# Optimization experiments

Measured on AMD Instinct MI355X. Metric: run time of the kernel, lower is better.

The kernel has to match this reference:

```python
import jax, jax.numpy as jnp
import numpy as np

B, S, D, H = 4, 2048, 1024, 16
DEPTH = D // H


def setup_inputs() -> dict:
    key = jax.random.key(0)
    ks = jax.random.split(key, 12)
    q = jax.random.normal(ks[0], (B, S, D), dtype=jnp.float32)
    k = jax.random.normal(ks[1], (B, S, D), dtype=jnp.float32)
    v = jax.random.normal(ks[2], (B, S, D), dtype=jnp.float32)
    # causal mask: 1.0 where attention is disallowed (upper triangle), per `mask * -1e9`
    mask = 1.0 - jnp.tril(jnp.ones((S, S), dtype=jnp.float32))
    mask = mask[None, None, :, :]  # [1,1,S,S] broadcastable over batch/heads
    scale = 1.0 / np.sqrt(D)
    Wq = jax.random.normal(ks[3], (D, D), dtype=jnp.float32) * scale
    Wk = jax.random.normal(ks[4], (D, D), dtype=jnp.float32) * scale
    Wv = jax.random.normal(ks[5], (D, D), dtype=jnp.float32) * scale
    Wo = jax.random.normal(ks[6], (D, D), dtype=jnp.float32) * scale
    bq = jnp.zeros((D,), jnp.float32)
    bk = jnp.zeros((D,), jnp.float32)
    bv = jnp.zeros((D,), jnp.float32)
    bo = jnp.zeros((D,), jnp.float32)
    return {"query": q, "key": k, "value": v, "mask": mask,
            "Wq": Wq, "bq": bq, "Wk": Wk, "bk": bk,
            "Wv": Wv, "bv": bv, "Wo": Wo, "bo": bo}


def _split_heads(x):
    # [B, S, D] -> [B, H, S, depth]
    b, s, _ = x.shape
    return x.reshape(b, s, H, DEPTH).transpose(0, 2, 1, 3)


def reference(query, key, value, mask, Wq, bq, Wk, bk, Wv, bv, Wo, bo):
    q = _split_heads(query @ Wq + bq)   # [B,H,S,depth]
    k = _split_heads(key @ Wk + bk)
    v = _split_heads(value @ Wv + bv)
    scores = jnp.einsum('bhqd,bhkd->bhqk', q, k) / jnp.sqrt(
        jnp.asarray(DEPTH, q.dtype))
    scores = scores + mask * (-1e9)
    attn = jax.nn.softmax(scores, axis=-1)
    out = jnp.einsum('bhqk,bhkd->bhqd', attn, v)   # [B,H,S,depth]
    out = out.transpose(0, 2, 1, 3).reshape(query.shape[0], -1, H * DEPTH)
    return out @ Wo + bo
```

## Files before the change

kernel.cpp:

```cpp
#include <hip/hip_runtime.h>

#define Bsz 4
#define SEQ 2048
#define DIM 1024
#define NH 16
#define HD 64

typedef float  f32x4  __attribute__((ext_vector_type(4)));
typedef __bf16 bf16x8 __attribute__((ext_vector_type(8)));
typedef __bf16 bf16x4 __attribute__((ext_vector_type(4)));
typedef short  s16x4  __attribute__((ext_vector_type(4)));

__device__ __forceinline__ f32x4 mfma16(bf16x8 a, bf16x8 b, f32x4 c) {
    return __builtin_amdgcn_mfma_f32_16x16x32_bf16(a, b, c, 0, 0, 0);
}
__device__ __forceinline__ f32x4 mfma16k16(bf16x4 a, bf16x4 b, f32x4 c) {
#if defined(__has_builtin) && __has_builtin(__builtin_amdgcn_mfma_f32_16x16x16bf16_1k)
    return __builtin_amdgcn_mfma_f32_16x16x16bf16_1k(
        __builtin_bit_cast(s16x4, a), __builtin_bit_cast(s16x4, b), c, 0, 0, 0);
#else
    asm volatile("s_nop 2\n\tv_mfma_f32_16x16x16_bf16 %0, %1, %2, %0\n\ts_nop 7\n\ts_nop 7"
                 : "+v"(c) : "v"(a), "v"(b));
    return c;
#endif
}

#define GLD_LDS16(gsrc, ldst)                                                        \
    __builtin_amdgcn_global_load_lds(                                                \
        (const __attribute__((address_space(1))) void*)(gsrc),                       \
        (__attribute__((address_space(3))) void*)(ldst), 16, 0, 0)

__global__ __launch_bounds__(256) void wt_kernel(
    const float* __restrict__ Wq, const float* __restrict__ Wk,
    const float* __restrict__ Wv, const float* __restrict__ Wo,
    __bf16* __restrict__ wt)
{
    __shared__ float tile[64][65];
    int z = blockIdx.z;
    const float* W = (z == 0) ? Wq : (z == 1) ? Wk : (z == 2) ? Wv : Wo;
    __bf16* out = wt + (size_t)z * DIM * DIM;
    int kb = blockIdx.x * 64, nb = blockIdx.y * 64;
    int t = threadIdx.x;
    int cidx = t & 63, ridx = t >> 6;
#pragma unroll
    for (int i = 0; i < 16; i++) {
        int r = ridx + i * 4;
        tile[r][cidx] = W[(size_t)(kb + r) * DIM + nb + cidx];
    }
    __syncthreads();
#pragma unroll
    for (int i = 0; i < 16; i++) {
        int r = ridx + i * 4;
        out[(size_t)(nb + r) * DIM + kb + cidx] = (__bf16)tile[cidx][r];
    }
}

__global__ __launch_bounds__(256, 2) void gemm_proj(
    const float* __restrict__ Xq, const float* __restrict__ Xk,
    const float* __restrict__ Xv, const __bf16* __restrict__ wt,
    const float* __restrict__ bq, const float* __restrict__ bk,
    const float* __restrict__ bv,
    __bf16* __restrict__ oq, __bf16* __restrict__ ok, __bf16* __restrict__ ovT)
{
    int z = blockIdx.z;
    const float*  X    = (z == 0) ? Xq : (z == 1) ? Xk : Xv;
    const float*  bias = (z == 0) ? bq : (z == 1) ? bk : bv;
    const __bf16* Bt   = wt + (size_t)z * DIM * DIM;

    __shared__ __align__(16) char smem[36864];
    __bf16* const Ab = (__bf16*)smem;
    __bf16* const Bb = (__bf16*)(smem + 16384);

    int m0 = blockIdx.x * 128, n0 = blockIdx.y * 128;
    int tid = threadIdx.x, lane = tid & 63, w = tid >> 6;
    int c = lane & 15, g = lane >> 4;
    int wm = (w >> 1) * 64, wn = (w & 1) * 64;

    f32x4 acc[4][4] = {};

    int ar = tid >> 1, ah = tid & 1;
    const float* aptr = X + (size_t)(m0 + ar) * DIM + ah * 16;
    int awo = ar * 32 + ah * 16;

    int brow0 = (w * 2) * 16 + (lane >> 2);
    int bcol  = (lane & 3) * 8;
    const __bf16* bptr0 = Bt + (size_t)(n0 + brow0) * DIM + bcol;
    const __bf16* bptr1 = bptr0 + (size_t)16 * DIM;
    int bwo0 = (w * 2) * 512;
    int bwo1 = (w * 2 + 1) * 512;

    {
        f32x4 f0 = *(const f32x4*)(aptr);
        f32x4 f1 = *(const f32x4*)(aptr + 4);
        f32x4 f2 = *(const f32x4*)(aptr + 8);
        f32x4 f3 = *(const f32x4*)(aptr + 12);
        GLD_LDS16(bptr0, Bb + bwo0);
        GLD_LDS16(bptr1, Bb + bwo1);
        bf16x8 b0, b1;
#pragma unroll
        for (int j = 0; j < 4; j++) {
            b0[j]     = (__bf16)f0[j];
            b0[4 + j] = (__bf16)f1[j];
            b1[j]     = (__bf16)f2[j];
            b1[4 + j] = (__bf16)f3[j];
        }
        *(bf16x8*)(Ab + awo)     = b0;
        *(bf16x8*)(Ab + awo + 8) = b1;
    }
    __syncthreads();

    int cur = 0;
    for (int kt = 0; kt < 32; ++kt) {
        int nxt = kt + 1;
        int nb = cur ^ 1;
        f32x4 f0, f1, f2, f3;
        if (nxt < 32) {
            const float* ap = aptr + nxt * 32;
            f0 = *(const f32x4*)(ap);
            f1 = *(const f32x4*)(ap + 4);
            f2 = *(const f32x4*)(ap + 8);
            f3 = *(const f32x4*)(ap + 12);
            GLD_LDS16(bptr0 + nxt * 32, Bb + nb * 4096 + bwo0);
            GLD_LDS16(bptr1 + nxt * 32, Bb + nb * 4096 + bwo1);
        }
        bf16x8 af[4], bf[4];
#pragma unroll
        for (int mf = 0; mf < 4; mf++)
            af[mf] = *(bf16x8*)&Ab[cur * 4096 + (wm + mf * 16 + c) * 32 + g * 8];
#pragma unroll
        for (int nf = 0; nf < 4; nf++)
            bf[nf] = *(bf16x8*)&Bb[cur * 4096 + (wn + nf * 16 + c) * 32 + g * 8];
#pragma unroll
        for (int mf = 0; mf < 4; mf++)
#pragma unroll
            for (int nf = 0; nf < 4; nf++)
                acc[mf][nf] = mfma16(af[mf], bf[nf], acc[mf][nf]);
        if (nxt < 32) {
            bf16x8 b0, b1;
#pragma unroll
            for (int j = 0; j < 4; j++) {
                b0[j]     = (__bf16)f0[j];
                b0[4 + j] = (__bf16)f1[j];
                b1[j]     = (__bf16)f2[j];
                b1[4 + j] = (__bf16)f3[j];
            }
            *(bf16x8*)(Ab + nb * 4096 + awo)     = b0;
            *(bf16x8*)(Ab + nb * 4096 + awo + 8) = b1;
        }
        __syncthreads();
        cur = nb;
    }

    if (z == 2) {
        __bf16* T = (__bf16*)smem + (size_t)w * 4608;
#pragma unroll
        for (int nf = 0; nf < 4; nf++) {
            int col = n0 + wn + nf * 16 + c;
            int d = nf * 16 + c;
            float bval = bias[col];
#pragma unroll
            for (int mf = 0; mf < 4; mf++) {
                int sl = mf * 16 + g * 4;
                bf16x4 pk;
#pragma unroll
                for (int r = 0; r < 4; r++) pk[r] = (__bf16)(acc[mf][nf][r] + bval);
                *(bf16x4*)&T[d * 72 + sl] = pk;
            }
        }
        int h = (n0 + wn) >> 6;
        int bb = m0 >> 11;
        int s_base = (m0 & (SEQ - 1)) + wm;
        int dd = lane >> 2;
        int ss = (lane & 3) * 8;
        size_t obase = ((size_t)(bb * NH + h) * HD) * SEQ;
#pragma unroll
        for (int dgrp = 0; dgrp < 4; dgrp++)
#pragma unroll
            for (int half = 0; half < 2; half++) {
                int d = dgrp * 16 + dd;
                int s = half * 32 + ss;
                bf16x8 vv = *(bf16x8*)&T[d * 72 + s];
                *(bf16x8*)&ovT[obase + (size_t)d * SEQ + s_base + s] = vv;
            }
    } else {
        __bf16* Out = (z == 0) ? oq : ok;
#pragma unroll
        for (int nf = 0; nf < 4; nf++) {
            int col = n0 + wn + nf * 16 + c;
            float bval = bias[col];
#pragma unroll
            for (int mf = 0; mf < 4; mf++) {
                int row = m0 + wm + mf * 16 + g * 4;
#pragma unroll
                for (int r = 0; r < 4; r++)
                    Out[(size_t)(row + r) * DIM + col] = (__bf16)(acc[mf][nf][r] + bval);
            }
        }
    }
}

#define QSCALE 0.180336880f

__global__ __launch_bounds__(256, 2) void fa_kernel(
    const __bf16* __restrict__ qp, const __bf16* __restrict__ kp,
    const __bf16* __restrict__ vpT, __bf16* __restrict__ op)
{
    int bz = blockIdx.x;
    int bh = bz & 63;
    int b = bh >> 4, h = bh & 15;
    int qt = 15 - (bz >> 6);
    int q0 = qt * 128;

    int tid = threadIdx.x, lane = tid & 63, w = tid >> 6;
    int c = lane & 15, g = lane >> 4;

    __shared__ __bf16 Kbuf[64 * 64];
    __shared__ __bf16 Vbuf[64 * 64];

    const int qb[2] = {q0 + w * 16, q0 + 64 + w * 16};

    bf16x8 qf[2][2];
#pragma unroll
    for (int nq = 0; nq < 2; nq++) {
        const __bf16* qbase = qp + (size_t)(b * SEQ + qb[nq] + c) * DIM + h * HD;
#pragma unroll
        for (int kc = 0; kc < 2; kc++) {
            bf16x8 raw = *(const bf16x8*)(qbase + kc * 32 + g * 8);
            bf16x8 sc;
#pragma unroll
            for (int j = 0; j < 8; j++) sc[j] = (__bf16)((float)raw[j] * QSCALE);
            qf[nq][kc] = sc;
        }
    }

    f32x4 acc[4][2] = {};
    float m_run[2] = {-1e30f, -1e30f};
    float l_run[2] = {0.f, 0.f};

    int r8 = tid >> 3, c8 = tid & 7;
    int sch = c8 ^ (r8 & 7);
    const __bf16* kbase = kp  + (size_t)(b * SEQ + r8) * DIM + h * HD + sch * 8;
    const __bf16* vbase = vpT + ((size_t)(b * NH + h) * HD + r8) * SEQ + sch * 8;
    __bf16* kdst0 = Kbuf + w * 512;
    __bf16* kdst1 = Kbuf + 2048 + w * 512;
    __bf16* vdst0 = Vbuf + w * 512;
    __bf16* vdst1 = Vbuf + 2048 + w * 512;

    int vb4[4];
#pragma unroll
    for (int mkey = 0; mkey < 4; mkey++)
        vb4[mkey] = c * 64 + (((2 * mkey + (g >> 1)) ^ (c & 7)) * 8) + (g & 1) * 4;

    int ktmax = (q0 >> 6) + 2;
    for (int kt = 0; kt < ktmax; ++kt) {
        GLD_LDS16(kbase + (size_t)kt * 64 * DIM, kdst0);
        GLD_LDS16(kbase + (size_t)(kt * 64 + 32) * DIM, kdst1);
        GLD_LDS16(vbase + kt * 64, vdst0);
        GLD_LDS16(vbase + kt * 64 + (size_t)32 * SEQ, vdst1);
        __syncthreads();

        bool need0 = (kt * 64 <= qb[0] + 15);
        int kb0 = kt * 64;

        f32x4 s[4][2] = {};
#pragma unroll
        for (int kc = 0; kc < 2; kc++) {
            bf16x8 kf[4];
#pragma unroll
            for (int mkey = 0; mkey < 4; mkey++)
                kf[mkey] = *(bf16x8*)&Kbuf[(mkey * 16 + c) * 64 + (((kc * 4 + g) ^ (c & 7)) * 8)];
#pragma unroll
            for (int mkey = 0; mkey < 4; mkey++) {
                if (need0) s[mkey][0] = mfma16(kf[mkey], qf[0][kc], s[mkey][0]);
                s[mkey][1] = mfma16(kf[mkey], qf[1][kc], s[mkey][1]);
            }
        }

        bf16x4 pf[4][2];
#pragma unroll
        for (int nq = 0; nq < 2; nq++) {
            if (nq == 0 && !need0) continue;
            int qg = qb[nq] + c;
            if (kb0 + 63 > qg) {
#pragma unroll
                for (int mkey = 0; mkey < 4; mkey++)
#pragma unroll
                    for (int r2 = 0; r2 < 4; r2++)
                        if (kb0 + mkey * 16 + g * 4 + r2 > qg) s[mkey][nq][r2] = -1e30f;
            }
            float pm0 = fmaxf(fmaxf(s[0][nq][0], s[0][nq][1]), fmaxf(s[0][nq][2], s[0][nq][3]));
            float pm1 = fmaxf(fmaxf(s[1][nq][0], s[1][nq][1]), fmaxf(s[1][nq][2], s[1][nq][3]));
            float pm2 = fmaxf(fmaxf(s[2][nq][0], s[2][nq][1]), fmaxf(s[2][nq][2], s[2][nq][3]));
            float pm3 = fmaxf(fmaxf(s[3][nq][0], s[3][nq][1]), fmaxf(s[3][nq][2], s[3][nq][3]));
            float pm = fmaxf(fmaxf(pm0, pm1), fmaxf(pm2, pm3));
            pm = fmaxf(pm, __shfl_xor(pm, 16));
            pm = fmaxf(pm, __shfl_xor(pm, 32));
            float mo = m_run[nq];
            float mn = fmaxf(mo, pm);
            m_run[nq] = mn;
            float scl = exp2f(mo - mn);
            l_run[nq] *= scl;
#pragma unroll
            for (int nf = 0; nf < 4; nf++) acc[nf][nq] *= scl;
            float rs = 0.f;
#pragma unroll
            for (int mkey = 0; mkey < 4; mkey++) {
                bf16x4 pk;
#pragma unroll
                for (int r2 = 0; r2 < 4; r2++) {
                    float p = exp2f(s[mkey][nq][r2] - mn);
                    rs += p;
                    pk[r2] = (__bf16)p;
                }
                pf[mkey][nq] = pk;
            }
            rs += __shfl_xor(rs, 16);
            rs += __shfl_xor(rs, 32);
            l_run[nq] += rs;
        }

#pragma unroll
        for (int mkey = 0; mkey < 4; mkey++) {
#pragma unroll
            for (int nf = 0; nf < 4; nf++) {
                bf16x4 vf = *(bf16x4*)&Vbuf[vb4[mkey] + nf * 1024];
                if (need0) acc[nf][0] = mfma16k16(vf, pf[mkey][0], acc[nf][0]);
                acc[nf][1] = mfma16k16(vf, pf[mkey][1], acc[nf][1]);
            }
        }
        __syncthreads();
    }

#pragma unroll
    for (int nq = 0; nq < 2; nq++) {
        float inv = 1.f / l_run[nq];
        int row = qb[nq] + c;
        __bf16* obase = op + (size_t)(b * SEQ + row) * DIM + h * HD + g * 4;
#pragma unroll
        for (int nf = 0; nf < 4; nf++) {
            bf16x4 pk;
#pragma unroll
            for (int r2 = 0; r2 < 4; r2++) pk[r2] = (__bf16)(acc[nf][nq][r2] * inv);
            *(bf16x4*)(obase + nf * 16) = pk;
        }
    }
}

__global__ __launch_bounds__(256, 2) void gemm_out(
    const __bf16* __restrict__ Ain, const __bf16* __restrict__ wt,
    const float* __restrict__ bias, float* __restrict__ Out)
{
    const __bf16* Bt = wt + (size_t)3 * DIM * DIM;

    __shared__ __bf16 Ab[2][4096];
    __shared__ __bf16 Bb[2][4096];

    int m0 = blockIdx.x * 128, n0 = blockIdx.y * 128;
    int tid = threadIdx.x, lane = tid & 63, w = tid >> 6;
    int c = lane & 15, g = lane >> 4;
    int wm = (w >> 1) * 64, wn = (w & 1) * 64;

    f32x4 acc[4][4] = {};

    int srow = (w * 2) * 16 + (lane >> 2);
    int scol = (lane & 3) * 8;
    const __bf16* aptr0 = Ain + (size_t)(m0 + srow) * DIM + scol;
    const __bf16* aptr1 = aptr0 + (size_t)16 * DIM;
    const __bf16* bptr0 = Bt + (size_t)(n0 + srow) * DIM + scol;
    const __bf16* bptr1 = bptr0 + (size_t)16 * DIM;
    int so0 = (w * 2) * 512;
    int so1 = (w * 2 + 1) * 512;

    GLD_LDS16(aptr0, Ab[0] + so0);
    GLD_LDS16(aptr1, Ab[0] + so1);
    GLD_LDS16(bptr0, Bb[0] + so0);
    GLD_LDS16(bptr1, Bb[0] + so1);
    __syncthreads();

    int cur = 0;
    for (int kt = 0; kt < 32; ++kt) {
        int nxt = kt + 1;
        int nb = cur ^ 1;
        if (nxt < 32) {
            int k0 = nxt * 32;
            GLD_LDS16(aptr0 + k0, Ab[nb] + so0);
            GLD_LDS16(aptr1 + k0, Ab[nb] + so1);
            GLD_LDS16(bptr0 + k0, Bb[nb] + so0);
            GLD_LDS16(bptr1 + k0, Bb[nb] + so1);
        }
        bf16x8 af[4], bf[4];
#pragma unroll
        for (int mf = 0; mf < 4; mf++)
            af[mf] = *(bf16x8*)&Ab[cur][(wm + mf * 16 + c) * 32 + g * 8];
#pragma unroll
        for (int nf = 0; nf < 4; nf++)
            bf[nf] = *(bf16x8*)&Bb[cur][(wn + nf * 16 + c) * 32 + g * 8];
#pragma unroll
        for (int mf = 0; mf < 4; mf++)
#pragma unroll
            for (int nf = 0; nf < 4; nf++)
                acc[mf][nf] = mfma16(af[mf], bf[nf], acc[mf][nf]);
        __syncthreads();
        cur = nb;
    }

#pragma unroll
    for (int nf = 0; nf < 4; nf++) {
        int col = n0 + wn + nf * 16 + c;
        float bval = bias[col];
#pragma unroll
        for (int mf = 0; mf < 4; mf++) {
            int row = m0 + wm + mf * 16 + g * 4;
#pragma unroll
            for (int r = 0; r < 4; r++)
                Out[(size_t)(row + r) * DIM + col] = acc[mf][nf][r] + bval;
        }
    }
}

extern "C" void kernel_launch(void* const* d_in, const int* in_sizes, int n_in,
                              void* d_out, int out_size, void* d_ws, size_t ws_size,
                              hipStream_t stream)
{
    const float* q  = (const float*)d_in[0];
    const float* k  = (const float*)d_in[1];
    const float* v  = (const float*)d_in[2];
    const float* Wq = (const float*)d_in[4];
    const float* bq = (const float*)d_in[5];
    const float* Wk = (const float*)d_in[6];
    const float* bk = (const float*)d_in[7];
    const float* Wv = (const float*)d_in[8];
    const float* bv = (const float*)d_in[9];
    const float* Wo = (const float*)d_in[10];
    const float* bo = (const float*)d_in[11];

    char* ws = (char*)d_ws;
    __bf16* wt  = (__bf16*)ws;
    __bf16* qp  = (__bf16*)(ws + (size_t)(8u  << 20));
    __bf16* kp  = (__bf16*)(ws + (size_t)(24u << 20));
    __bf16* vpT = (__bf16*)(ws + (size_t)(40u << 20));
    __bf16* ao  = (__bf16*)(ws + (size_t)(56u << 20));

    wt_kernel<<<dim3(16, 16, 4), 256, 0, stream>>>(Wq, Wk, Wv, Wo, wt);
    gemm_proj<<<dim3(64, 8, 3), 256, 0, stream>>>(q, k, v, wt, bq, bk, bv, qp, kp, vpT);
    fa_kernel<<<dim3(1024), 256, 0, stream>>>(qp, kp, vpT, ao);
    gemm_out<<<dim3(64, 8), 256, 0, stream>>>(ao, wt, bo, (float*)d_out);

    (void)in_sizes; (void)n_in; (void)out_size; (void)ws_size;
}
```

Before: 201.1 us.

## Pre-convert activations to bf16 and load projection GEMM operands via LDS DMA

Adds a separate kernel that converts the fp32 q/k/v activations to bf16 in the workspace. A new projection GEMM then streams both operands straight into LDS with global_load_lds, with no register round-trip or in-loop conversion. The V output's transposed write is also reworked to go through a smaller LDS staging tile with vectorized stores. The cost is an extra launch plus a write and re-read of 48 MB of bf16 activations. The old fp32 path is kept as a fallback when the workspace is too small.

```diff
diff --git a/kernel.cpp b/kernel.cpp
--- a/kernel.cpp
+++ b/kernel.cpp
@@ -30,6 +30,23 @@
         (const __attribute__((address_space(1))) void*)(gsrc),                       \
         (__attribute__((address_space(3))) void*)(ldst), 16, 0, 0)
 
+__global__ __launch_bounds__(256) void cvt_kernel(
+    const float* __restrict__ x0, const float* __restrict__ x1,
+    const float* __restrict__ x2,
+    __bf16* __restrict__ o0, __bf16* __restrict__ o1, __bf16* __restrict__ o2)
+{
+    int z = blockIdx.y;
+    const float* X = (z == 0) ? x0 : (z == 1) ? x1 : x2;
+    __bf16*      O = (z == 0) ? o0 : (z == 1) ? o1 : o2;
+    size_t i = ((size_t)blockIdx.x * 256 + threadIdx.x) * 8;
+    f32x4 a = *(const f32x4*)(X + i);
+    f32x4 b = *(const f32x4*)(X + i + 4);
+    bf16x8 r;
+#pragma unroll
+    for (int j = 0; j < 4; j++) { r[j] = (__bf16)a[j]; r[4 + j] = (__bf16)b[j]; }
+    *(bf16x8*)(O + i) = r;
+}
+
 __global__ __launch_bounds__(256) void wt_kernel(
     const float* __restrict__ Wq, const float* __restrict__ Wk,
     const float* __restrict__ Wv, const float* __restrict__ Wo,
@@ -56,6 +73,119 @@
 }
 
 __global__ __launch_bounds__(256, 2) void gemm_proj(
+    const __bf16* __restrict__ Xq, const __bf16* __restrict__ Xk,
+    const __bf16* __restrict__ Xv, const __bf16* __restrict__ wt,
+    const float* __restrict__ bq, const float* __restrict__ bk,
+    const float* __restrict__ bv,
+    __bf16* __restrict__ oq, __bf16* __restrict__ ok, __bf16* __restrict__ ovT)
+{
+    int z = blockIdx.z;
+    const __bf16* X    = (z == 0) ? Xq : (z == 1) ? Xk : Xv;
+    const float*  bias = (z == 0) ? bq : (z == 1) ? bk : bv;
+    const __bf16* Bt   = wt + (size_t)z * DIM * DIM;
+
+    __shared__ __align__(16) char smem[32768];
+    __bf16* const Ab = (__bf16*)smem;
+    __bf16* const Bb = (__bf16*)(smem + 16384);
+
+    int m0 = blockIdx.x * 128, n0 = blockIdx.y * 128;
+    int tid = threadIdx.x, lane = tid & 63, w = tid >> 6;
+    int c = lane & 15, g = lane >> 4;
+    int wm = (w >> 1) * 64, wn = (w & 1) * 64;
+
+    f32x4 acc[4][4] = {};
+
+    int srow = (w * 2) * 16 + (lane >> 2);
+    int scol = (lane & 3) * 8;
+    const __bf16* aptr0 = X + (size_t)(m0 + srow) * DIM + scol;
+    const __bf16* aptr1 = aptr0 + (size_t)16 * DIM;
+    const __bf16* bptr0 = Bt + (size_t)(n0 + srow) * DIM + scol;
+    const __bf16* bptr1 = bptr0 + (size_t)16 * DIM;
+    int so0 = (w * 2) * 512;
+    int so1 = (w * 2 + 1) * 512;
+
+    GLD_LDS16(aptr0, Ab + so0);
+    GLD_LDS16(aptr1, Ab + so1);
+    GLD_LDS16(bptr0, Bb + so0);
+    GLD_LDS16(bptr1, Bb + so1);
+    __syncthreads();
+
+    int cur = 0;
+    for (int kt = 0; kt < 32; ++kt) {
+        int nxt = kt + 1;
+        int nb = cur ^ 1;
+        if (nxt < 32) {
+            int k0 = nxt * 32;
+            GLD_LDS16(aptr0 + k0, Ab + nb * 4096 + so0);
+            GLD_LDS16(aptr1 + k0, Ab + nb * 4096 + so1);
+            GLD_LDS16(bptr0 + k0, Bb + nb * 4096 + so0);
+            GLD_LDS16(bptr1 + k0, Bb + nb * 4096 + so1);
+        }
+        bf16x8 af[4], bf[4];
+#pragma unroll
+        for (int mf = 0; mf < 4; mf++)
+            af[mf] = *(bf16x8*)&Ab[cur * 4096 + (wm + mf * 16 + c) * 32 + g * 8];
+#pragma unroll
+        for (int nf = 0; nf < 4; nf++)
+            bf[nf] = *(bf16x8*)&Bb[cur * 4096 + (wn + nf * 16 + c) * 32 + g * 8];
+#pragma unroll
+        for (int mf = 0; mf < 4; mf++)
+#pragma unroll
+            for (int nf = 0; nf < 4; nf++)
+                acc[mf][nf] = mfma16(af[mf], bf[nf], acc[mf][nf]);
+        __syncthreads();
+        cur = nb;
+    }
+
+    if (z == 2) {
+        __bf16* T = (__bf16*)smem + (size_t)w * 2304;
+        int h = (n0 + wn) >> 6;
+        int bb = m0 >> 11;
+        int s_base = (m0 & (SEQ - 1)) + wm;
+        int dd = lane >> 2;
+        int ss = (lane & 3) * 8;
+        size_t obase = ((size_t)(bb * NH + h) * HD) * SEQ;
+#pragma unroll
+        for (int half = 0; half < 2; half++) {
+#pragma unroll
+            for (int mh = 0; mh < 2; mh++) {
+                int mf = half * 2 + mh;
+#pragma unroll
+                for (int nf = 0; nf < 4; nf++) {
+                    int col = n0 + wn + nf * 16 + c;
+                    int d = nf * 16 + c;
+                    float bval = bias[col];
+                    bf16x4 pk;
+#pragma unroll
+                    for (int r = 0; r < 4; r++) pk[r] = (__bf16)(acc[mf][nf][r] + bval);
+                    *(bf16x4*)&T[d * 36 + mh * 16 + g * 4] = pk;
+                }
+            }
+#pragma unroll
+            for (int dgrp = 0; dgrp < 4; dgrp++) {
+                int d = dgrp * 16 + dd;
+                bf16x8 vv = *(bf16x8*)&T[d * 36 + ss];
+                *(bf16x8*)&ovT[obase + (size_t)d * SEQ + s_base + half * 32 + ss] = vv;
+            }
+        }
+    } else {
+        __bf16* Out = (z == 0) ? oq : ok;
+#pragma unroll
+        for (int nf = 0; nf < 4; nf++) {
+            int col = n0 + wn + nf * 16 + c;
+            float bval = bias[col];
+#pragma unroll
+            for (int mf = 0; mf < 4; mf++) {
+                int row = m0 + wm + mf * 16 + g * 4;
+#pragma unroll
+                for (int r = 0; r < 4; r++)
+                    Out[(size_t)(row + r) * DIM + col] = (__bf16)(acc[mf][nf][r] + bval);
+            }
+        }
+    }
+}
+
+__global__ __launch_bounds__(256, 2) void gemm_proj_f32(
     const float* __restrict__ Xq, const float* __restrict__ Xk,
     const float* __restrict__ Xv, const __bf16* __restrict__ wt,
     const float* __restrict__ bq, const float* __restrict__ bk,
@@ -99,10 +229,8 @@
         bf16x8 b0, b1;
 #pragma unroll
         for (int j = 0; j < 4; j++) {
-            b0[j]     = (__bf16)f0[j];
-            b0[4 + j] = (__bf16)f1[j];
-            b1[j]     = (__bf16)f2[j];
-            b1[4 + j] = (__bf16)f3[j];
+            b0[j] = (__bf16)f0[j]; b0[4 + j] = (__bf16)f1[j];
+            b1[j] = (__bf16)f2[j]; b1[4 + j] = (__bf16)f3[j];
         }
         *(bf16x8*)(Ab + awo)     = b0;
         *(bf16x8*)(Ab + awo + 8) = b1;
@@ -139,10 +267,8 @@
             bf16x8 b0, b1;
 #pragma unroll
             for (int j = 0; j < 4; j++) {
-                b0[j]     = (__bf16)f0[j];
-                b0[4 + j] = (__bf16)f1[j];
-                b1[j]     = (__bf16)f2[j];
-                b1[4 + j] = (__bf16)f3[j];
+                b0[j] = (__bf16)f0[j]; b0[4 + j] = (__bf16)f1[j];
+                b1[j] = (__bf16)f2[j]; b1[4 + j] = (__bf16)f3[j];
             }
             *(bf16x8*)(Ab + nb * 4096 + awo)     = b0;
             *(bf16x8*)(Ab + nb * 4096 + awo + 8) = b1;
@@ -440,11 +566,19 @@
     __bf16* kp  = (__bf16*)(ws + (size_t)(24u << 20));
     __bf16* vpT = (__bf16*)(ws + (size_t)(40u << 20));
     __bf16* ao  = (__bf16*)(ws + (size_t)(56u << 20));
+    __bf16* xq  = (__bf16*)(ws + (size_t)(72u << 20));
+    __bf16* xk  = (__bf16*)(ws + (size_t)(88u << 20));
+    __bf16* xv  = (__bf16*)(ws + (size_t)(104u << 20));
 
     wt_kernel<<<dim3(16, 16, 4), 256, 0, stream>>>(Wq, Wk, Wv, Wo, wt);
-    gemm_proj<<<dim3(64, 8, 3), 256, 0, stream>>>(q, k, v, wt, bq, bk, bv, qp, kp, vpT);
+    if (ws_size >= ((size_t)120u << 20)) {
+        cvt_kernel<<<dim3(4096, 3), 256, 0, stream>>>(q, k, v, xq, xk, xv);
+        gemm_proj<<<dim3(64, 8, 3), 256, 0, stream>>>(xq, xk, xv, wt, bq, bk, bv, qp, kp, vpT);
+    } else {
+        gemm_proj_f32<<<dim3(64, 8, 3), 256, 0, stream>>>(q, k, v, wt, bq, bk, bv, qp, kp, vpT);
+    }
     fa_kernel<<<dim3(1024), 256, 0, stream>>>(qp, kp, vpT, ao);
     gemm_out<<<dim3(64, 8), 256, 0, stream>>>(ao, wt, bo, (float*)d_out);
 
-    (void)in_sizes; (void)n_in; (void)out_size; (void)ws_size;
-}
+    (void)in_sizes; (void)n_in; (void)out_size;
+}
```

New measurement: 203.5 us. About the same (+1.2%).
